# Kernel tuning notes

Hardware: AMD Instinct MI355X
Metric: run time of the kernel (lower is better)

The kernel has to match this reference:

```python
import jax, jax.numpy as jnp
from jax import lax
import numpy as np

T = 100  # number of binarization thresholds, as in nn.Module (linspace(0,1,100))
THRESHOLDS = jnp.linspace(0.0, 1.0, T)


def _count_components(binimg):
    """4-connected component count per image via iterative min-label propagation.
    binimg: [N,H,W] float in {0,1}. Returns [N] int32 component counts.
    Equivalent math to the source's recursive DFS flood fill, vectorized."""
    N, H, W = binimg.shape
    fg = binimg > 0
    BIG = H * W  # sentinel label for background
    idx = jnp.arange(H * W, dtype=jnp.int32).reshape(H, W)
    lab0 = jnp.where(fg, idx[None], jnp.int32(BIG))

    def prop(lab):
        p = jnp.pad(lab, ((0, 0), (1, 1), (1, 1)), constant_values=BIG)
        nmin = jnp.minimum(jnp.minimum(p[:, :-2, 1:-1], p[:, 2:, 1:-1]),
                           jnp.minimum(p[:, 1:-1, :-2], p[:, 1:-1, 2:]))
        return jnp.where(fg, jnp.minimum(lab, nmin), jnp.int32(BIG))

    def cond(c):
        return ~c[1]

    def body(c):
        lab = c[0]
        new = prop(prop(prop(lab)))  # 3 propagation steps per convergence check
        return (new, jnp.all(new == lab))

    lab, _ = lax.while_loop(cond, body, (lab0, jnp.array(False)))
    # each component keeps exactly one pixel whose label equals its own index
    return jnp.sum(fg & (lab == idx[None]), axis=(1, 2)).astype(jnp.int32)


def _betti(prob):
    """prob: [R,H,W] -> [T,R,2] (b0, b1) per threshold per region.
    b1 = b0 - euler, euler = #pixels - #4-neighbor edges (as in source)."""
    R, H, W = prob.shape
    binz = (prob[None] > THRESHOLDS[:, None, None, None]).astype(jnp.float32)  # [T,R,H,W]
    flat = binz.reshape(T * R, H, W)
    b0 = lax.stop_gradient(_count_components(flat)).astype(jnp.float32).reshape(T, R)
    pix = flat.sum((1, 2))
    edges = (flat[:, :-1] * flat[:, 1:]).sum((1, 2)) + (flat[:, :, :-1] * flat[:, :, 1:]).sum((1, 2))
    euler = (pix - edges).reshape(T, R)
    b1 = b0 - euler
    return jnp.stack([b0, b1], axis=-1)  # [T,R,2]


def setup_inputs() -> dict:
    key = jax.random.key(0)
    k1, k2 = jax.random.split(key)
    three_class_prob = jax.random.uniform(k1, (4, 3, 128, 128), dtype=jnp.float32)
    selected_regions = jnp.arange(4, dtype=jnp.int64)
    gt_barcodes = jax.random.uniform(k2, (4, 6, T - 1, 2), dtype=jnp.float32)
    return {"three_class_prob": three_class_prob,
            "selected_regions": selected_regions,
            "gt_barcodes": gt_barcodes}


def reference(three_class_prob, selected_regions, gt_barcodes):
    sel = three_class_prob[selected_regions]  # [R,3,H,W]
    inside = _betti(sel[:, 0])     # channel 0
    boundary = _betti(sel[:, 1])   # channel 1
    union = inside                 # source uses channel 0:1 again -> same values
    codes = jnp.concatenate([inside, boundary, union], axis=-1)  # [T,R,6]
    # barcode extraction: birth at increases of the betti curve, death at decreases
    d = codes[1:] - codes[:-1]                 # [T-1,R,6]
    th = THRESHOLDS[:-1, None, None]
    birth = jnp.where(d > 0, th, 0.0)
    death = jnp.where(d < 0, th, 0.0)
    barcodes = jnp.stack([birth, death], axis=-1).transpose(1, 2, 0, 3)  # [R,6,T-1,2]
    # fixed-shape matching: pair barcodes sorted by birth time (Hungarian surrogate)
    ord_b = jnp.argsort(barcodes[..., 0], axis=-1)
    ord_g = jnp.argsort(gt_barcodes[..., 0], axis=-1)
    bs = jnp.take_along_axis(barcodes, ord_b[..., None], axis=-2)
    gs = jnp.take_along_axis(gt_barcodes, ord_g[..., None], axis=-2)
    matched_diff = jnp.sum(jnp.abs(bs - gs), axis=-1)                  # [R,6,T-1]
    unmatched_len = jnp.sum(barcodes[..., 1] - barcodes[..., 0], axis=-1)  # [R,6]
    return jnp.mean(matched_diff) + jnp.mean(unmatched_len)
```

## Files before the change

### kernel.cpp

```cpp
#include <hip/hip_runtime.h>

typedef unsigned long long u64;

#define FLAG_M1 0x13579BDFu
#define FLAG_M2 0x2468ACE1u
#define WL_CAP  4928

__device__ __forceinline__ int find_root(int* L, int a){
    int p = L[a];
    while(p != a){
        int gp = L[p];
        if(gp != p) L[a] = gp;
        a = p; p = gp;
    }
    return a;
}

__device__ __forceinline__ int unite(int* L, int a, int b){
    while(true){
        a = find_root(L, a);
        b = find_root(L, b);
        if(a == b) return 0;
        int hi = (a > b) ? a : b;
        int lo = (a > b) ? b : a;
        int old = atomicCAS(&L[hi], hi, lo);
        if(old == hi) return 1;
        a = old; b = lo;
    }
}

__device__ __forceinline__ void ccl_body(const float* __restrict__ prob,
                                         const int*   __restrict__ sel,
                                         float*       __restrict__ betti,
                                         unsigned*    __restrict__ flags,
                                         float*       __restrict__ out,
                                         u64* M, u64* S, int* Pr, int* L,
                                         unsigned* WL, int* red,
                                         int tid, int bid){
    if(bid == 0 && tid == 0) atomicExch(out, 0.0f);
    const int ch = bid / 400, t = (bid % 400) >> 2, r = bid & 3;
    const float th = (float)t / 99.0f;
    const float* img = prob + (size_t)(sel[r] * 3 + ch) * 16384;

    const int w = tid;
    {
        const float4* imgv = (const float4*)img;
        u64 mw = 0ULL;
        #pragma unroll
        for(int k = 0; k < 16; k++){
            const float4 v = imgv[w * 16 + k];
            const unsigned nib = (unsigned)(v.x > th)
                               | ((unsigned)(v.y > th) << 1)
                               | ((unsigned)(v.z > th) << 2)
                               | ((unsigned)(v.w > th) << 3);
            mw |= (u64)nib << (4 * k);
        }
        M[w] = mw;
    }
    __syncthreads();

    const int lane = tid & 63, wave = tid >> 6;
    const int row = w >> 1, half = w & 1;
    const u64 m = M[w];
    const u64 lcar = half ? (M[w - 1] >> 63) : 0ULL;
    const u64 s = m & ~((m << 1) | lcar);
    S[w] = s;
    int pix   = __popcll(m);
    int edges = __popcll(m & ((m << 1) | lcar));
    const u64 va = (row > 0) ? M[w - 2] : 0ULL;
    edges += __popcll(m & va);
    const int runs = __popcll(s);
    u64 csm = 0ULL;
    if(row > 0){
        const u64 c = m & va;
        const u64 ccar = half ? ((M[w - 1] & M[w - 3]) >> 63) : 0ULL;
        csm = c & ~((c << 1) | ccar);
    }
    const int nseg = __popcll(csm);

    const int packed = runs | (nseg << 16);
    int incl = packed;
    for(int off = 1; off < 64; off <<= 1){
        int n = __shfl_up(incl, off, 64);
        if(lane >= off) incl += n;
    }
    if(lane == 63) red[wave] = incl;
    __syncthreads();
    int woff = 0;
    for(int k = 0; k < wave; k++) woff += red[k];
    const int exclP = woff + incl - packed;
    Pr[w] = exclP;
    if(w == 255) Pr[256] = exclP + packed;
    const u64 sa = (row > 0) ? S[w - 2] : 0ULL;
    __syncthreads();
    const int RK = Pr[256];
    const int R  = RK & 0xFFFF;
    const int K  = (int)((unsigned)RK >> 16);
    const int excl  = exclP & 0xFFFF;
    const int sexcl = (int)((unsigned)exclP >> 16);
    const int Pa = (row > 0) ? (Pr[w - 2] & 0xFFFF) : 0;

    {
        int4* L4 = (int4*)L;
        const int n4 = (R + 3) >> 2;
        for(int i = tid; i < n4; i += 256){ int b = i * 4; L4[i] = make_int4(b, b+1, b+2, b+3); }
    }
    {
        int slot = sexcl;
        u64 cs = csm;
        while(cs && slot < WL_CAP){
            const int x = __ffsll(cs) - 1;
            cs &= cs - 1;
            const u64 lm = (2ULL << x) - 1;
            const int nb = excl + __popcll(s  & lm) - 1;
            const int na = Pa   + __popcll(sa & lm) - 1;
            WL[slot++] = ((unsigned)na << 13) | (unsigned)nb;
        }
    }
    __syncthreads();

    int merges = 0;
    {
        const int KC = (K < WL_CAP) ? K : WL_CAP;
        for(int i = tid; i < KC; i += 256){
            const unsigned e = WL[i];
            merges += unite(L, (int)(e >> 13), (int)(e & 0x1FFFu));
        }
        if(K > WL_CAP){
            u64 cs = csm; int idx = sexcl;
            while(cs){
                const int x = __ffsll(cs) - 1;
                cs &= cs - 1;
                if(idx >= WL_CAP){
                    const u64 lm = (2ULL << x) - 1;
                    const int nb = excl + __popcll(s  & lm) - 1;
                    const int na = Pa   + __popcll(sa & lm) - 1;
                    merges += unite(L, na, nb);
                }
                idx++;
            }
        }
    }

    int v0 = pix, v1 = edges, v2 = merges;
    for(int off = 32; off; off >>= 1){
        v0 += __shfl_down(v0, off, 64);
        v1 += __shfl_down(v1, off, 64);
        v2 += __shfl_down(v2, off, 64);
    }
    __syncthreads();
    if(lane == 0){ red[wave*3] = v0; red[wave*3+1] = v1; red[wave*3+2] = v2; }
    __syncthreads();
    if(tid == 0){
        int P = 0, E = 0, MG = 0;
        for(int k = 0; k < 4; k++){ P += red[k*3]; E += red[k*3+1]; MG += red[k*3+2]; }
        const float b0f = (float)(R - MG);
        const float b1f = b0f - ((float)P - (float)E);
        const size_t o = (((size_t)ch * 100 + t) * 4 + r) * 2;
        __hip_atomic_store(&betti[o],     b0f, __ATOMIC_RELAXED, __HIP_MEMORY_SCOPE_AGENT);
        __hip_atomic_store(&betti[o + 1], b1f, __ATOMIC_RELAXED, __HIP_MEMORY_SCOPE_AGENT);
        unsigned* f = flags + (size_t)bid * 8;
        __hip_atomic_store(&f[0], FLAG_M1, __ATOMIC_RELEASE, __HIP_MEMORY_SCOPE_AGENT);
        __hip_atomic_store(&f[4], FLAG_M2, __ATOMIC_RELEASE, __HIP_MEMORY_SCOPE_AGENT);
    }
}

__device__ __forceinline__ void rows_body(const float* __restrict__ betti,
                                          const float* __restrict__ gt,
                                          float*       __restrict__ out,
                                          int row, int tid, float* fsh){
    float* codes = fsh;
    float* birth = fsh + 100;
    float* bs0   = fsh + 199;
    float* bs1   = fsh + 298;
    float* gs0   = fsh + 397;
    float* gs1   = fsh + 496;
    float* gsh   = fsh + 595;
    float* redf  = fsh + 793;
    const int r = row / 6, j = row % 6;
    const int chmap[6] = {0, 0, 1, 1, 0, 0};
    const int ch = chmap[j], comp = j & 1;

    if(tid < 100)
        codes[tid] = __hip_atomic_load(&betti[(((size_t)ch * 100 + tid) * 4 + r) * 2 + comp],
                                       __ATOMIC_RELAXED, __HIP_MEMORY_SCOPE_AGENT);
    const float* g = gt + (size_t)row * 198;
    for(int i = tid; i < 198; i += 256) gsh[i] = g[i];
    __syncthreads();

    float b = 0.f, d = 0.f;
    if(tid < 99){
        const float dv = codes[tid + 1] - codes[tid];
        const float thv = (float)tid / 99.0f;
        b = (dv > 0.f) ? thv : 0.f;
        d = (dv < 0.f) ? thv : 0.f;
        birth[tid] = b;
    }
    __syncthreads();

    if(tid < 99){
        int zb = 0, tz = 0;
        for(int k = 0; k < 99; k++){
            const int z = (birth[k] == 0.f) ? 1 : 0;
            tz += z;
            if(k < tid) zb += z;
        }
        const int pos = (b == 0.f) ? zb : (tz + tid - zb);
        bs0[pos] = b; bs1[pos] = d;

        const float gb = gsh[tid * 2];
        int rank = 0;
        for(int k = 0; k < 99; k++){
            const float o = gsh[k * 2];
            rank += (o < gb || (o == gb && k < tid)) ? 1 : 0;
        }
        gs0[rank] = gb; gs1[rank] = gsh[tid * 2 + 1];
    }
    __syncthreads();

    float mm = 0.f, u = 0.f;
    if(tid < 99){
        mm = fabsf(bs0[tid] - gs0[tid]) + fabsf(bs1[tid] - gs1[tid]);
        u = d - b;
    }
    for(int off = 32; off; off >>= 1){
        mm += __shfl_down(mm, off, 64);
        u  += __shfl_down(u,  off, 64);
    }
    if((tid & 63) == 0){ redf[(tid >> 6) * 2] = mm; redf[(tid >> 6) * 2 + 1] = u; }
    __syncthreads();
    if(tid == 0)
        atomicAdd(out, (redf[0] + redf[2] + redf[4] + redf[6]) / 2376.0f
                     + (redf[1] + redf[3] + redf[5] + redf[7]) / 24.0f);
}

__global__ __launch_bounds__(256) void fused_kernel(const float* __restrict__ prob,
                                                    const int*   __restrict__ sel,
                                                    const float* __restrict__ gt,
                                                    float*       __restrict__ betti,
                                                    unsigned*    __restrict__ flags,
                                                    float*       __restrict__ out){
    __shared__ u64 M[256];
    __shared__ u64 S[256];
    __shared__ int Pr[257];
    __shared__ int L[6400];
    __shared__ unsigned WL[WL_CAP];
    __shared__ int red[12];
    const int tid = threadIdx.x, bid = blockIdx.x;

    if(bid < 800){
        ccl_body(prob, sel, betti, flags, out, M, S, Pr, L, WL, red, tid, bid);
        return;
    }

    const int row = bid - 800;
    const int r = row / 6, j = row % 6;
    const int chmap[6] = {0, 0, 1, 1, 0, 0};
    const int ch = chmap[j];

    if(tid <= 100){
        const int pb = (tid < 100) ? (ch * 400 + tid * 4 + r) : 0;
        unsigned* f = flags + (size_t)pb * 8;
        while(__hip_atomic_load(&f[0], __ATOMIC_ACQUIRE, __HIP_MEMORY_SCOPE_AGENT) != FLAG_M1 ||
              __hip_atomic_load(&f[4], __ATOMIC_ACQUIRE, __HIP_MEMORY_SCOPE_AGENT) != FLAG_M2){
            __builtin_amdgcn_s_sleep(8);
        }
    }
    __syncthreads();

    rows_body(betti, gt, out, row, tid, (float*)L);
}

extern "C" void kernel_launch(void* const* d_in, const int* in_sizes, int n_in,
                              void* d_out, int out_size, void* d_ws, size_t ws_size,
                              hipStream_t stream){
    const float* prob = (const float*)d_in[0];
    const int*   sel  = (const int*)d_in[1];
    const float* gt   = (const float*)d_in[2];
    float*    betti = (float*)d_ws;
    unsigned* flags = (unsigned*)((char*)d_ws + 8192);

    fused_kernel<<<824, 256, 0, stream>>>(prob, sel, gt, betti, flags, (float*)d_out);
}
```

Measured before the change: 93.83 us.

## Replace atomicCAS union-find with iterative hook-and-compress rounds over worklist

Merges in the shared-memory union-find now run as synchronous rounds. Each round finds roots without path compression, hooks the higher root to the lower with atomicMin, then does a block-wide pointer-jumping pass, repeating until no thread hooks. The component count is taken by counting self-rooted labels rather than counting successful CAS merges. The aim is to avoid CAS retry loops and contention, at the cost of several block-wide barriers and full-array compress passes per round.

```diff
diff --git a/kernel.cpp b/kernel.cpp
--- a/kernel.cpp
+++ b/kernel.cpp
@@ -16,15 +16,15 @@
     return a;
 }
 
-__device__ __forceinline__ int unite(int* L, int a, int b){
+__device__ __forceinline__ void unite(int* L, int a, int b){
     while(true){
         a = find_root(L, a);
         b = find_root(L, b);
-        if(a == b) return 0;
+        if(a == b) return;
         int hi = (a > b) ? a : b;
         int lo = (a > b) ? b : a;
         int old = atomicCAS(&L[hi], hi, lo);
-        if(old == hi) return 1;
+        if(old == hi) return;
         a = old; b = lo;
     }
 }
@@ -119,13 +119,8 @@
     }
     __syncthreads();
 
-    int merges = 0;
     {
         const int KC = (K < WL_CAP) ? K : WL_CAP;
-        for(int i = tid; i < KC; i += 256){
-            const unsigned e = WL[i];
-            merges += unite(L, (int)(e >> 13), (int)(e & 0x1FFFu));
-        }
         if(K > WL_CAP){
             u64 cs = csm; int idx = sexcl;
             while(cs){
@@ -135,14 +130,36 @@
                     const u64 lm = (2ULL << x) - 1;
                     const int nb = excl + __popcll(s  & lm) - 1;
                     const int na = Pa   + __popcll(sa & lm) - 1;
-                    merges += unite(L, na, nb);
+                    unite(L, na, nb);
                 }
                 idx++;
             }
         }
-    }
-
-    int v0 = pix, v1 = edges, v2 = merges;
+        while(true){
+            int hooked = 0;
+            for(int i = tid; i < KC; i += 256){
+                const unsigned e = WL[i];
+                int a = (int)(e >> 13), b = (int)(e & 0x1FFFu);
+                int p;
+                while((p = L[a]) != a) a = p;
+                while((p = L[b]) != b) b = p;
+                if(a != b){
+                    hooked = 1;
+                    const int hi = (a > b) ? a : b;
+                    const int lo = a ^ b ^ hi;
+                    atomicMin(&L[hi], lo);
+                }
+            }
+            if(__syncthreads_count(hooked) == 0) break;
+            for(int i = tid; i < R; i += 256) L[i] = L[L[i]];
+            __syncthreads();
+        }
+    }
+
+    int roots = 0;
+    for(int i = tid; i < R; i += 256) roots += (L[i] == i) ? 1 : 0;
+
+    int v0 = pix, v1 = edges, v2 = roots;
     for(int off = 32; off; off >>= 1){
         v0 += __shfl_down(v0, off, 64);
         v1 += __shfl_down(v1, off, 64);
@@ -152,9 +169,9 @@
     if(lane == 0){ red[wave*3] = v0; red[wave*3+1] = v1; red[wave*3+2] = v2; }
     __syncthreads();
     if(tid == 0){
-        int P = 0, E = 0, MG = 0;
-        for(int k = 0; k < 4; k++){ P += red[k*3]; E += red[k*3+1]; MG += red[k*3+2]; }
-        const float b0f = (float)(R - MG);
+        int P = 0, E = 0, B0 = 0;
+        for(int k = 0; k < 4; k++){ P += red[k*3]; E += red[k*3+1]; B0 += red[k*3+2]; }
+        const float b0f = (float)B0;
         const float b1f = b0f - ((float)P - (float)E);
         const size_t o = (((size_t)ch * 100 + t) * 4 + r) * 2;
         __hip_atomic_store(&betti[o],     b0f, __ATOMIC_RELAXED, __HIP_MEMORY_SCOPE_AGENT);
```

After: 123.0 us. 1.31x slower.
